# Kernel tuning notes

Hardware: AMD Instinct MI355X
Metric: run time of the kernel (lower is better)

The kernel has to match this reference:

```python
import jax, jax.numpy as jnp
import numpy as np

B, L, D = 4, 2048, 1024
H = 16
HD = D // H


def setup_inputs() -> dict:
    key = jax.random.key(0)
    ks = jax.random.split(key, 6)
    x = jax.random.normal(ks[0], (B, L, D), dtype=jnp.float32)
    # True = masked-out (strict upper triangle -> causal)
    causal_mask = jnp.triu(jnp.ones((L, L), dtype=bool), k=1)
    key_padding_mask = jnp.zeros((B, L), dtype=bool)  # no padding
    lim = 1.0 / np.sqrt(D)
    Wqkv = jax.random.uniform(ks[1], (3 * D, D), minval=-lim, maxval=lim, dtype=jnp.float32)
    bqkv = jax.random.uniform(ks[2], (3 * D,), minval=-lim, maxval=lim, dtype=jnp.float32)
    Wproj = jax.random.uniform(ks[3], (D, D), minval=-lim, maxval=lim, dtype=jnp.float32)
    bproj = jax.random.uniform(ks[4], (D,), minval=-lim, maxval=lim, dtype=jnp.float32)
    return {"x": x, "causal_mask": causal_mask, "key_padding_mask": key_padding_mask,
            "Wqkv": Wqkv, "bqkv": bqkv, "Wproj": Wproj, "bproj": bproj}


def reference(x, causal_mask, key_padding_mask, Wqkv, bqkv, Wproj, bproj):
    b, l, d = x.shape
    scale = (d // H // 1) ** 0  # placeholder; real scale below
    scale = (d // H) ** -0.5
    qkv = x @ Wqkv.T + bqkv                      # [B,L,3D]
    qkv = qkv.reshape(b, l, 3, H, HD).transpose(2, 0, 3, 1, 4)  # [3,B,H,L,HD]
    q, k, v = qkv[0], qkv[1], qkv[2]
    attn = jnp.einsum('bhqd,bhkd->bhqk', q, k) * scale          # [B,H,L,L]
    neg_inf = jnp.float32(-jnp.inf)
    attn = jnp.where(causal_mask[None, None, :, :], neg_inf, attn)
    attn = jnp.where(key_padding_mask[:, None, None, :], neg_inf, attn)
    attn = jax.nn.softmax(attn, axis=-1)
    attn = jnp.nan_to_num(attn, nan=0.0, posinf=0.0, neginf=0.0)
    out = jnp.einsum('bhqk,bhkd->bhqd', attn, v)                # [B,H,L,HD]
    out = out.transpose(0, 2, 1, 3).reshape(b, l, d)
    return out @ Wproj.T + bproj
```

## Files before the change

kernel.cpp:

```cpp
#include <hip/hip_runtime.h>

typedef __bf16 bf16;
typedef __attribute__((ext_vector_type(8))) __bf16 bf16x8;
typedef __attribute__((ext_vector_type(4))) __bf16 bf16x4;
typedef __attribute__((ext_vector_type(4))) float f32x4;
typedef __attribute__((ext_vector_type(4))) short short4v;

#define AS1C(p) ((const __attribute__((address_space(1))) void*)(p))
#define AS3(p)  ((__attribute__((address_space(3))) void*)(p))

static __device__ __forceinline__ f32x4 pv_mfma(bf16x4 a, bf16x4 b, f32x4 c) {
#if __has_builtin(__builtin_amdgcn_mfma_f32_16x16x16bf16_1k)
  return __builtin_amdgcn_mfma_f32_16x16x16bf16_1k(
      __builtin_bit_cast(short4v, a), __builtin_bit_cast(short4v, b), c, 0, 0, 0);
#else
  f32x4 d = c;
  asm("v_mfma_f32_16x16x16_bf16 %0, %1, %2, %0" : "+v"(d) : "v"(a), "v"(b));
  return d;
#endif
}

__global__ void castk(const float* __restrict__ in, bf16* __restrict__ out, long n) {
  long i = ((long)blockIdx.x * blockDim.x + threadIdx.x) * 4;
  if (i >= n) return;
  f32x4 v = *reinterpret_cast<const f32x4*>(in + i);
  bf16x4 o;
  o[0] = (bf16)v[0]; o[1] = (bf16)v[1]; o[2] = (bf16)v[2]; o[3] = (bf16)v[3];
  *reinterpret_cast<bf16x4*>(out + i) = o;
}

template<int MODE>
__global__ __launch_bounds__(256, 2)
void gemm_bt(const bf16* __restrict__ A, const bf16* __restrict__ BT,
             const float* __restrict__ bias, void* __restrict__ Cout,
             int M, int N, int K) {
  __shared__ bf16 As[128 * 64];
  __shared__ bf16 Bs[128 * 64];
  const int tid = threadIdx.x;
  const int lane = tid & 63;
  const int w = tid >> 6;
  const int wm = w >> 1, wn = w & 1;
  const int row0 = blockIdx.y * 128, col0 = blockIdx.x * 128;

  f32x4 acc[4][4] = {};

  const int srow = tid >> 3;
  const int scb = ((tid & 7) << 4) ^ ((srow & 7) << 4);
  const long aoff = (long)(row0 + srow) * K + (scb >> 1);
  const long boff = (long)(col0 + srow) * K + (scb >> 1);

  for (int k0 = 0; k0 < K; k0 += 64) {
    #pragma unroll
    for (int i = 0; i < 4; ++i) {
      __builtin_amdgcn_global_load_lds(AS1C(A + aoff + (long)i * 32 * K + k0),
                                       AS3((char*)As + i * 4096 + w * 1024), 16, 0, 0);
      __builtin_amdgcn_global_load_lds(AS1C(BT + boff + (long)i * 32 * K + k0),
                                       AS3((char*)Bs + i * 4096 + w * 1024), 16, 0, 0);
    }
    __syncthreads();
    #pragma unroll
    for (int kf = 0; kf < 2; ++kf) {
      bf16x8 af[4], bfr[4];
      #pragma unroll
      for (int m = 0; m < 4; ++m) {
        int r = wm * 64 + m * 16 + (lane & 15);
        int cb = (kf * 64 + ((lane >> 4) << 4)) ^ ((r & 7) << 4);
        af[m] = *reinterpret_cast<const bf16x8*>((const char*)As + r * 128 + cb);
      }
      #pragma unroll
      for (int n = 0; n < 4; ++n) {
        int r = wn * 64 + n * 16 + (lane & 15);
        int cb = (kf * 64 + ((lane >> 4) << 4)) ^ ((r & 7) << 4);
        bfr[n] = *reinterpret_cast<const bf16x8*>((const char*)Bs + r * 128 + cb);
      }
      #pragma unroll
      for (int m = 0; m < 4; ++m)
        #pragma unroll
        for (int n = 0; n < 4; ++n) {
          if constexpr (MODE == 1)
            acc[m][n] = __builtin_amdgcn_mfma_f32_16x16x32_bf16(bfr[n], af[m], acc[m][n], 0, 0, 0);
          else
            acc[m][n] = __builtin_amdgcn_mfma_f32_16x16x32_bf16(af[m], bfr[n], acc[m][n], 0, 0, 0);
        }
    }
    __syncthreads();
  }

  const int g = lane >> 4, q = lane & 15;

  if constexpr (MODE == 0) {
    #pragma unroll
    for (int m = 0; m < 4; ++m)
      #pragma unroll
      for (int n = 0; n < 4; ++n)
        #pragma unroll
        for (int r = 0; r < 4; ++r) {
          int grow = row0 + wm * 64 + m * 16 + g * 4 + r;
          int gcol = col0 + wn * 64 + n * 16 + q;
          reinterpret_cast<float*>(Cout)[(long)grow * N + gcol] = acc[m][n][r] + bias[gcol];
        }
  } else if constexpr (MODE == 1) {
    const int t = (int)blockIdx.x >> 3;
    const int h = (((int)blockIdx.x << 1) | wn) & 15;
    const float qs = (t == 0) ? 0.125f : 1.0f;
    bf16* outb = reinterpret_cast<bf16*>(Cout) + (t ? 8388608 : 0);
    #pragma unroll
    for (int n = 0; n < 4; ++n) {
      f32x4 bv = *reinterpret_cast<const f32x4*>(bias + col0 + wn * 64 + n * 16 + g * 4);
      #pragma unroll
      for (int m = 0; m < 4; ++m) {
        int grow = row0 + wm * 64 + m * 16 + q;
        int bb = grow >> 11, ll = grow & 2047;
        bf16x4 o;
        #pragma unroll
        for (int r = 0; r < 4; ++r) o[r] = (bf16)((acc[m][n][r] + bv[r]) * qs);
        *reinterpret_cast<bf16x4*>(outb + ((long)(bb * 16 + h) * 2048 + ll) * 64 + n * 16 + g * 4) = o;
      }
    }
  } else {
    const int h = (((int)blockIdx.x << 1) | wn) & 15;
    bf16* outb = reinterpret_cast<bf16*>(Cout);
    #pragma unroll
    for (int n = 0; n < 4; ++n) {
      float bv = bias[col0 + wn * 64 + n * 16 + q];
      int hd = n * 16 + q;
      #pragma unroll
      for (int m = 0; m < 4; ++m) {
        int grow = row0 + wm * 64 + m * 16 + g * 4;
        int bb = grow >> 11, ll = grow & 2047;
        bf16x4 o;
        #pragma unroll
        for (int r = 0; r < 4; ++r) o[r] = (bf16)(acc[m][n][r] + bv);
        *reinterpret_cast<bf16x4*>(outb + ((long)(bb * 16 + h) * 64 + hd) * 2048 + ll) = o;
      }
    }
  }
}

__global__ __launch_bounds__(256, 4)
void attn_fwd(const bf16* __restrict__ Qg, const bf16* __restrict__ Kg,
              const bf16* __restrict__ VTg, bf16* __restrict__ Og) {
  __shared__ bf16 Ks[2][64 * 64];
  __shared__ bf16 Vs[2][64 * 64];
  const int tid = threadIdx.x, lane = tid & 63, w = tid >> 6;
  const int g = lane >> 4, q = lane & 15;

  const int orig = blockIdx.x;
  const int wgid = (orig & 7) * 256 + (orig >> 3);
  const int bh = wgid >> 5;
  const int qi = 31 - (wgid & 31);
  const int bb = bh >> 4, h = bh & 15;
  const long base = (long)bh * (2048 * 64);
  const int qw = qi * 64 + w * 16;
  const int myq = qw + q;

  bf16x8 qf[2];
  qf[0] = *reinterpret_cast<const bf16x8*>(Qg + base + (long)myq * 64 + g * 8);
  qf[1] = *reinterpret_cast<const bf16x8*>(Qg + base + (long)myq * 64 + 32 + g * 8);

  f32x4 accO[4] = {};
  float m = -1e30f, l = 0.f;

  const int srow = tid >> 3;
  const int scb = ((tid & 7) << 4) ^ ((srow & 7) << 4);
  const int nt = qi + 1;

  auto stage = [&](int kt, int buf) {
    #pragma unroll
    for (int i = 0; i < 2; ++i) {
      __builtin_amdgcn_global_load_lds(
          AS1C(Kg + base + (long)(kt * 64 + i * 32 + srow) * 64 + (scb >> 1)),
          AS3((char*)&Ks[buf][0] + i * 4096 + w * 1024), 16, 0, 0);
      __builtin_amdgcn_global_load_lds(
          AS1C(VTg + base + (long)(i * 32 + srow) * 2048 + kt * 64 + (scb >> 1)),
          AS3((char*)&Vs[buf][0] + i * 4096 + w * 1024), 16, 0, 0);
    }
  };

  stage(0, 0);

  for (int kt = 0; kt < nt; ++kt) {
    const int cur = kt & 1;
    __syncthreads();
    if (kt + 1 < nt) stage(kt + 1, cur ^ 1);

    const char* Kb = (const char*)&Ks[cur][0];
    const char* Vb = (const char*)&Vs[cur][0];

    f32x4 sT[4] = {};
    #pragma unroll
    for (int kf = 0; kf < 2; ++kf) {
      #pragma unroll
      for (int a = 0; a < 4; ++a) {
        int r = a * 16 + q;
        int cb = (kf * 64 + g * 16) ^ ((r & 7) << 4);
        bf16x8 kb = *reinterpret_cast<const bf16x8*>(Kb + r * 128 + cb);
        sT[a] = __builtin_amdgcn_mfma_f32_16x16x32_bf16(kb, qf[kf], sT[a], 0, 0, 0);
      }
    }

    if (kt == qi) {
      #pragma unroll
      for (int a = 0; a < 4; ++a)
        #pragma unroll
        for (int r = 0; r < 4; ++r) {
          int kv = kt * 64 + a * 16 + 4 * g + r;
          if (kv > myq) sT[a][r] = -1e30f;
        }
    }

    float vm = -1e30f;
    #pragma unroll
    for (int a = 0; a < 4; ++a)
      #pragma unroll
      for (int r = 0; r < 4; ++r) vm = fmaxf(vm, sT[a][r]);
    vm = fmaxf(vm, __shfl_xor(vm, 16));
    vm = fmaxf(vm, __shfl_xor(vm, 32));
    float mnew = fmaxf(m, vm);
    float fac = __expf(m - mnew);
    m = mnew;

    float ps = 0.f;
    bf16x4 pa[4];
    #pragma unroll
    for (int a = 0; a < 4; ++a)
      #pragma unroll
      for (int r = 0; r < 4; ++r) {
        float p = __expf(sT[a][r] - mnew);
        ps += p;
        pa[a][r] = (bf16)p;
      }
    ps += __shfl_xor(ps, 16);
    ps += __shfl_xor(ps, 32);
    l = l * fac + ps;
    #pragma unroll
    for (int b = 0; b < 4; ++b) accO[b] *= fac;

    #pragma unroll
    for (int a = 0; a < 4; ++a) {
      #pragma unroll
      for (int b = 0; b < 4; ++b) {
        int row = b * 16 + q;
        int cb = (a * 32 + g * 8) ^ ((row & 7) << 4);
        bf16x4 vfrag = *reinterpret_cast<const bf16x4*>(Vb + row * 128 + cb);
        accO[b] = pv_mfma(vfrag, pa[a], accO[b]);
      }
    }
  }

  __syncthreads();
  char* ob = (char*)&Ks[0][0] + w * 2048;
  float rl = 1.0f / l;
  #pragma unroll
  for (int b = 0; b < 4; ++b)
    #pragma unroll
    for (int r = 0; r < 4; ++r) {
      int hd = 16 * b + 4 * g + r;
      int cb = (hd * 2) ^ ((q & 7) << 4);
      *reinterpret_cast<bf16*>(ob + q * 128 + cb) = (bf16)(accO[b][r] * rl);
    }
  asm volatile("s_waitcnt lgkmcnt(0)" ::: "memory");
  __builtin_amdgcn_sched_barrier(0);

  const int rr = lane >> 2, cc = lane & 3;
  #pragma unroll
  for (int half = 0; half < 2; ++half) {
    int hd0 = cc * 16 + half * 8;
    int cb = (hd0 * 2) ^ ((rr & 7) << 4);
    bf16x8 vv = *reinterpret_cast<const bf16x8*>(ob + rr * 128 + cb);
    *reinterpret_cast<bf16x8*>(Og + (long)(bb * 2048 + qw + rr) * 1024 + h * 64 + hd0) = vv;
  }
}

extern "C" void kernel_launch(void* const* d_in, const int* in_sizes, int n_in,
                              void* d_out, int out_size, void* d_ws, size_t ws_size,
                              hipStream_t stream) {
  (void)in_sizes; (void)n_in; (void)out_size; (void)ws_size;
  const float* x     = (const float*)d_in[0];
  const float* Wqkv  = (const float*)d_in[3];
  const float* bqkv  = (const float*)d_in[4];
  const float* Wproj = (const float*)d_in[5];
  const float* bproj = (const float*)d_in[6];

  bf16* xb     = (bf16*)d_ws;
  bf16* Wqkvb  = xb + 8388608;
  bf16* Wprojb = Wqkvb + 3145728;
  bf16* Qb     = Wprojb + 1048576;
  bf16* Ob     = Qb + 3 * 8388608;

  castk<<<8192, 256, 0, stream>>>(x, xb, 8388608);
  castk<<<3072, 256, 0, stream>>>(Wqkv, Wqkvb, 3145728);
  castk<<<1024, 256, 0, stream>>>(Wproj, Wprojb, 1048576);

  gemm_bt<1><<<dim3(16, 64), 256, 0, stream>>>(xb, Wqkvb, bqkv, (void*)Qb, 8192, 3072, 1024);
  gemm_bt<2><<<dim3(8, 64), 256, 0, stream>>>(xb, Wqkvb + (long)2048 * 1024, bqkv + 2048,
                                              (void*)(Qb + 16777216), 8192, 3072, 1024);

  attn_fwd<<<dim3(2048), 256, 0, stream>>>(Qb, Qb + 8388608, Qb + 16777216, Ob);

  gemm_bt<0><<<dim3(8, 64), 256, 0, stream>>>(Ob, Wprojb, bproj, d_out, 8192, 1024, 1024);
}
```

Baseline: 196.4 us.

## Process 128 queries per attention block with two row tiles per wave and lazy rescale

The attention kernel now handles 128 query rows per workgroup, with each wave owning two 16-row tiles that share every K/V fragment read from LDS. This halves the grid and the K/V staging traffic per query. The softmax switches to exp2 with log2(e) folded into the Q scale in the QKV GEMM, and it rescales the running max only when it grows by more than 8 (a lazy rescale). MFMA sections are wrapped in s_setprio. The cost is higher register pressure from doubled accumulators, and waves whose first tile is fully masked sit idle on the last tiles.

```diff
diff --git a/kernel.cpp b/kernel.cpp
--- a/kernel.cpp
+++ b/kernel.cpp
@@ -18,6 +18,17 @@
   asm("v_mfma_f32_16x16x16_bf16 %0, %1, %2, %0" : "+v"(d) : "v"(a), "v"(b));
   return d;
 #endif
+}
+
+static __device__ __forceinline__ float fexp2(float x) {
+#if __has_builtin(__builtin_amdgcn_exp2f)
+  return __builtin_amdgcn_exp2f(x);
+#else
+  return exp2f(x);
+#endif
+}
+static __device__ __forceinline__ float m3(float a, float b, float c) {
+  return fmaxf(fmaxf(a, b), c);
 }
 
 __global__ void castk(const float* __restrict__ in, bf16* __restrict__ out, long n) {
@@ -102,7 +113,7 @@
   } else if constexpr (MODE == 1) {
     const int t = (int)blockIdx.x >> 3;
     const int h = (((int)blockIdx.x << 1) | wn) & 15;
-    const float qs = (t == 0) ? 0.125f : 1.0f;
+    const float qs = (t == 0) ? 0.125f * 1.44269504f : 1.0f;
     bf16* outb = reinterpret_cast<bf16*>(Cout) + (t ? 8388608 : 0);
     #pragma unroll
     for (int n = 0; n < 4; ++n) {
@@ -146,24 +157,30 @@
   const int g = lane >> 4, q = lane & 15;
 
   const int orig = blockIdx.x;
-  const int wgid = (orig & 7) * 256 + (orig >> 3);
-  const int bh = wgid >> 5;
-  const int qi = 31 - (wgid & 31);
+  const int wgid = (orig & 7) * 128 + (orig >> 3);
+  const int bh = wgid >> 4;
+  const int qi = 15 - (wgid & 15);
   const int bb = bh >> 4, h = bh & 15;
   const long base = (long)bh * (2048 * 64);
-  const int qw = qi * 64 + w * 16;
-  const int myq = qw + q;
-
-  bf16x8 qf[2];
-  qf[0] = *reinterpret_cast<const bf16x8*>(Qg + base + (long)myq * 64 + g * 8);
-  qf[1] = *reinterpret_cast<const bf16x8*>(Qg + base + (long)myq * 64 + 32 + g * 8);
-
-  f32x4 accO[4] = {};
-  float m = -1e30f, l = 0.f;
+  const int q0 = qi * 128;
+  const int qw0 = q0 + w * 32, qw1 = qw0 + 16;
+  const int myq0 = qw0 + q, myq1 = qw1 + q;
+
+  const bf16* Qp = Qg + base;
+  bf16x8 qf0[2], qf1[2];
+  qf0[0] = *reinterpret_cast<const bf16x8*>(Qp + (long)myq0 * 64 + g * 8);
+  qf0[1] = *reinterpret_cast<const bf16x8*>(Qp + (long)myq0 * 64 + 32 + g * 8);
+  qf1[0] = *reinterpret_cast<const bf16x8*>(Qp + (long)myq1 * 64 + g * 8);
+  qf1[1] = *reinterpret_cast<const bf16x8*>(Qp + (long)myq1 * 64 + 32 + g * 8);
+
+  f32x4 accO0[4] = {}, accO1[4] = {};
+  float m0 = -1e30f, l0 = 0.f, m1 = -1e30f, l1 = 0.f;
 
   const int srow = tid >> 3;
   const int scb = ((tid & 7) << 4) ^ ((srow & 7) << 4);
-  const int nt = qi + 1;
+  const int nt = 2 * qi + 2;
+  const int ntw0 = ((qw0 + 15) >> 6) + 1;
+  const int ntw1 = ((qw1 + 15) >> 6) + 1;
 
   auto stage = [&](int kt, int buf) {
     #pragma unroll
@@ -177,98 +194,165 @@
     }
   };
 
+  auto osm = [&](f32x4 (&sT)[4], float& m, float& l, f32x4 (&accO)[4], bf16x4 (&pa)[4]) {
+    float t0 = m3(sT[0][0], sT[0][1], sT[0][2]);
+    float t1 = m3(sT[0][3], sT[1][0], sT[1][1]);
+    float t2 = m3(sT[1][2], sT[1][3], sT[2][0]);
+    float t3 = m3(sT[2][1], sT[2][2], sT[2][3]);
+    float t4 = m3(sT[3][0], sT[3][1], sT[3][2]);
+    float vm = fmaxf(m3(t0, t1, t2), m3(t3, t4, sT[3][3]));
+    vm = fmaxf(vm, __shfl_xor(vm, 16));
+    vm = fmaxf(vm, __shfl_xor(vm, 32));
+    if (__ballot(vm > m + 8.0f)) {
+      float mnew = fmaxf(m, vm);
+      float fac = fexp2(m - mnew);
+      m = mnew;
+      #pragma unroll
+      for (int b = 0; b < 4; ++b) accO[b] *= fac;
+      l *= fac;
+    }
+    float ps = 0.f;
+    #pragma unroll
+    for (int a = 0; a < 4; ++a)
+      #pragma unroll
+      for (int r = 0; r < 4; ++r) {
+        float p = fexp2(sT[a][r] - m);
+        ps += p;
+        pa[a][r] = (bf16)p;
+      }
+    ps += __shfl_xor(ps, 16);
+    ps += __shfl_xor(ps, 32);
+    l += ps;
+  };
+
   stage(0, 0);
 
   for (int kt = 0; kt < nt; ++kt) {
     const int cur = kt & 1;
     __syncthreads();
     if (kt + 1 < nt) stage(kt + 1, cur ^ 1);
+    if (kt >= ntw1) continue;
 
     const char* Kb = (const char*)&Ks[cur][0];
     const char* Vb = (const char*)&Vs[cur][0];
-
-    f32x4 sT[4] = {};
-    #pragma unroll
-    for (int kf = 0; kf < 2; ++kf) {
-      #pragma unroll
-      for (int a = 0; a < 4; ++a) {
-        int r = a * 16 + q;
-        int cb = (kf * 64 + g * 16) ^ ((r & 7) << 4);
-        bf16x8 kb = *reinterpret_cast<const bf16x8*>(Kb + r * 128 + cb);
-        sT[a] = __builtin_amdgcn_mfma_f32_16x16x32_bf16(kb, qf[kf], sT[a], 0, 0, 0);
-      }
-    }
-
-    if (kt == qi) {
+    const bool both = kt < ntw0;
+
+    f32x4 sT0[4] = {}, sT1[4] = {};
+    __builtin_amdgcn_s_setprio(1);
+    if (both) {
+      #pragma unroll
+      for (int kf = 0; kf < 2; ++kf)
+        #pragma unroll
+        for (int a = 0; a < 4; ++a) {
+          int r = a * 16 + q;
+          int cb = (kf * 64 + g * 16) ^ ((r & 7) << 4);
+          bf16x8 kb = *reinterpret_cast<const bf16x8*>(Kb + r * 128 + cb);
+          sT0[a] = __builtin_amdgcn_mfma_f32_16x16x32_bf16(kb, qf0[kf], sT0[a], 0, 0, 0);
+          sT1[a] = __builtin_amdgcn_mfma_f32_16x16x32_bf16(kb, qf1[kf], sT1[a], 0, 0, 0);
+        }
+    } else {
+      #pragma unroll
+      for (int kf = 0; kf < 2; ++kf)
+        #pragma unroll
+        for (int a = 0; a < 4; ++a) {
+          int r = a * 16 + q;
+          int cb = (kf * 64 + g * 16) ^ ((r & 7) << 4);
+          bf16x8 kb = *reinterpret_cast<const bf16x8*>(Kb + r * 128 + cb);
+          sT1[a] = __builtin_amdgcn_mfma_f32_16x16x32_bf16(kb, qf1[kf], sT1[a], 0, 0, 0);
+        }
+    }
+    __builtin_amdgcn_s_setprio(0);
+
+    if (kt * 64 + 63 > qw1) {
       #pragma unroll
       for (int a = 0; a < 4; ++a)
         #pragma unroll
         for (int r = 0; r < 4; ++r) {
           int kv = kt * 64 + a * 16 + 4 * g + r;
-          if (kv > myq) sT[a][r] = -1e30f;
-        }
-    }
-
-    float vm = -1e30f;
-    #pragma unroll
-    for (int a = 0; a < 4; ++a)
-      #pragma unroll
-      for (int r = 0; r < 4; ++r) vm = fmaxf(vm, sT[a][r]);
-    vm = fmaxf(vm, __shfl_xor(vm, 16));
-    vm = fmaxf(vm, __shfl_xor(vm, 32));
-    float mnew = fmaxf(m, vm);
-    float fac = __expf(m - mnew);
-    m = mnew;
-
-    float ps = 0.f;
-    bf16x4 pa[4];
-    #pragma unroll
-    for (int a = 0; a < 4; ++a)
+          if (kv > myq1) sT1[a][r] = -1e30f;
+        }
+    }
+    if (both && kt * 64 + 63 > qw0) {
+      #pragma unroll
+      for (int a = 0; a < 4; ++a)
+        #pragma unroll
+        for (int r = 0; r < 4; ++r) {
+          int kv = kt * 64 + a * 16 + 4 * g + r;
+          if (kv > myq0) sT0[a][r] = -1e30f;
+        }
+    }
+
+    bf16x4 pa0[4], pa1[4];
+    if (both) osm(sT0, m0, l0, accO0, pa0);
+    osm(sT1, m1, l1, accO1, pa1);
+
+    __builtin_amdgcn_s_setprio(1);
+    if (both) {
+      #pragma unroll
+      for (int a = 0; a < 4; ++a)
+        #pragma unroll
+        for (int b = 0; b < 4; ++b) {
+          int row = b * 16 + q;
+          int cb = (a * 32 + g * 8) ^ ((row & 7) << 4);
+          bf16x4 vfrag = *reinterpret_cast<const bf16x4*>(Vb + row * 128 + cb);
+          accO0[b] = pv_mfma(vfrag, pa0[a], accO0[b]);
+          accO1[b] = pv_mfma(vfrag, pa1[a], accO1[b]);
+        }
+    } else {
+      #pragma unroll
+      for (int a = 0; a < 4; ++a)
+        #pragma unroll
+        for (int b = 0; b < 4; ++b) {
+          int row = b * 16 + q;
+          int cb = (a * 32 + g * 8) ^ ((row & 7) << 4);
+          bf16x4 vfrag = *reinterpret_cast<const bf16x4*>(Vb + row * 128 + cb);
+          accO1[b] = pv_mfma(vfrag, pa1[a], accO1[b]);
+        }
+    }
+    __builtin_amdgcn_s_setprio(0);
+  }
+
+  __syncthreads();
+  char* lds0 = (char*)&Ks[0][0];
+  {
+    char* ob = lds0 + (w * 2 + 0) * 2048;
+    float rl = 1.0f / l0;
+    #pragma unroll
+    for (int b = 0; b < 4; ++b)
       #pragma unroll
       for (int r = 0; r < 4; ++r) {
-        float p = __expf(sT[a][r] - mnew);
-        ps += p;
-        pa[a][r] = (bf16)p;
-      }
-    ps += __shfl_xor(ps, 16);
-    ps += __shfl_xor(ps, 32);
-    l = l * fac + ps;
-    #pragma unroll
-    for (int b = 0; b < 4; ++b) accO[b] *= fac;
-
-    #pragma unroll
-    for (int a = 0; a < 4; ++a) {
-      #pragma unroll
-      for (int b = 0; b < 4; ++b) {
-        int row = b * 16 + q;
-        int cb = (a * 32 + g * 8) ^ ((row & 7) << 4);
-        bf16x4 vfrag = *reinterpret_cast<const bf16x4*>(Vb + row * 128 + cb);
-        accO[b] = pv_mfma(vfrag, pa[a], accO[b]);
-      }
-    }
-  }
-
-  __syncthreads();
-  char* ob = (char*)&Ks[0][0] + w * 2048;
-  float rl = 1.0f / l;
-  #pragma unroll
-  for (int b = 0; b < 4; ++b)
-    #pragma unroll
-    for (int r = 0; r < 4; ++r) {
-      int hd = 16 * b + 4 * g + r;
-      int cb = (hd * 2) ^ ((q & 7) << 4);
-      *reinterpret_cast<bf16*>(ob + q * 128 + cb) = (bf16)(accO[b][r] * rl);
-    }
+        int hd = 16 * b + 4 * g + r;
+        int cb = (hd * 2) ^ ((q & 7) << 4);
+        *reinterpret_cast<bf16*>(ob + q * 128 + cb) = (bf16)(accO0[b][r] * rl);
+      }
+  }
+  {
+    char* ob = lds0 + (w * 2 + 1) * 2048;
+    float rl = 1.0f / l1;
+    #pragma unroll
+    for (int b = 0; b < 4; ++b)
+      #pragma unroll
+      for (int r = 0; r < 4; ++r) {
+        int hd = 16 * b + 4 * g + r;
+        int cb = (hd * 2) ^ ((q & 7) << 4);
+        *reinterpret_cast<bf16*>(ob + q * 128 + cb) = (bf16)(accO1[b][r] * rl);
+      }
+  }
   asm volatile("s_waitcnt lgkmcnt(0)" ::: "memory");
   __builtin_amdgcn_sched_barrier(0);
 
   const int rr = lane >> 2, cc = lane & 3;
   #pragma unroll
-  for (int half = 0; half < 2; ++half) {
-    int hd0 = cc * 16 + half * 8;
-    int cb = (hd0 * 2) ^ ((rr & 7) << 4);
-    bf16x8 vv = *reinterpret_cast<const bf16x8*>(ob + rr * 128 + cb);
-    *reinterpret_cast<bf16x8*>(Og + (long)(bb * 2048 + qw + rr) * 1024 + h * 64 + hd0) = vv;
+  for (int s = 0; s < 2; ++s) {
+    char* ob = lds0 + (w * 2 + s) * 2048;
+    int qrow = qw0 + s * 16 + rr;
+    #pragma unroll
+    for (int half = 0; half < 2; ++half) {
+      int hd0 = cc * 16 + half * 8;
+      int cb = (hd0 * 2) ^ ((rr & 7) << 4);
+      bf16x8 vv = *reinterpret_cast<const bf16x8*>(ob + rr * 128 + cb);
+      *reinterpret_cast<bf16x8*>(Og + (long)(bb * 2048 + qrow) * 1024 + h * 64 + hd0) = vv;
+    }
   }
 }
 
@@ -296,7 +380,7 @@
   gemm_bt<2><<<dim3(8, 64), 256, 0, stream>>>(xb, Wqkvb + (long)2048 * 1024, bqkv + 2048,
                                               (void*)(Qb + 16777216), 8192, 3072, 1024);
 
-  attn_fwd<<<dim3(2048), 256, 0, stream>>>(Qb, Qb + 8388608, Qb + 16777216, Ob);
+  attn_fwd<<<dim3(1024), 256, 0, stream>>>(Qb, Qb + 8388608, Qb + 16777216, Ob);
 
   gemm_bt<0><<<dim3(8, 64), 256, 0, stream>>>(Ob, Wprojb, bproj, d_out, 8192, 1024, 1024);
 }
```

Measured after the change: 211.9 us. 1.08x slower.

## Share K/V tiles across 128-query attention blocks, use exp2 and lazy rescaling

Applied to the files above, without the earlier changes.

The attention kernel now runs 512-thread workgroups that cover 128 queries, so each staged K/V tile is shared by eight waves instead of four and the number of tile loads drops. Waves skip compute for tiles past their own causal limit but still take part in staging and barriers. The softmax uses exp2, with log2(e) folded into the Q scaling inside the QKV GEMM epilogue. It rescales the accumulator only when the running max rises by more than 8, and it raises wave priority around the MFMA sections and uses a three-input max tree. The launch bounds now request 8 waves per EU, which may force register pressure or spills, and idle waves on diagonal tiles add imbalance.

```diff
diff --git a/kernel.cpp b/kernel.cpp
--- a/kernel.cpp
+++ b/kernel.cpp
@@ -18,6 +18,17 @@
   asm("v_mfma_f32_16x16x16_bf16 %0, %1, %2, %0" : "+v"(d) : "v"(a), "v"(b));
   return d;
 #endif
+}
+
+static __device__ __forceinline__ float fexp2(float x) {
+#if __has_builtin(__builtin_amdgcn_exp2f)
+  return __builtin_amdgcn_exp2f(x);
+#else
+  return exp2f(x);
+#endif
+}
+static __device__ __forceinline__ float m3(float a, float b, float c) {
+  return fmaxf(fmaxf(a, b), c);
 }
 
 __global__ void castk(const float* __restrict__ in, bf16* __restrict__ out, long n) {
@@ -102,7 +113,7 @@
   } else if constexpr (MODE == 1) {
     const int t = (int)blockIdx.x >> 3;
     const int h = (((int)blockIdx.x << 1) | wn) & 15;
-    const float qs = (t == 0) ? 0.125f : 1.0f;
+    const float qs = (t == 0) ? 0.125f * 1.44269504f : 1.0f;
     bf16* outb = reinterpret_cast<bf16*>(Cout) + (t ? 8388608 : 0);
     #pragma unroll
     for (int n = 0; n < 4; ++n) {
@@ -137,7 +148,7 @@
   }
 }
 
-__global__ __launch_bounds__(256, 4)
+__global__ __launch_bounds__(512, 8)
 void attn_fwd(const bf16* __restrict__ Qg, const bf16* __restrict__ Kg,
               const bf16* __restrict__ VTg, bf16* __restrict__ Og) {
   __shared__ bf16 Ks[2][64 * 64];
@@ -146,12 +157,13 @@
   const int g = lane >> 4, q = lane & 15;
 
   const int orig = blockIdx.x;
-  const int wgid = (orig & 7) * 256 + (orig >> 3);
-  const int bh = wgid >> 5;
-  const int qi = 31 - (wgid & 31);
+  const int wgid = (orig & 7) * 128 + (orig >> 3);
+  const int bh = wgid >> 4;
+  const int qi = 15 - (wgid & 15);
   const int bb = bh >> 4, h = bh & 15;
   const long base = (long)bh * (2048 * 64);
-  const int qw = qi * 64 + w * 16;
+  const int q0 = qi * 128;
+  const int qw = q0 + w * 16;
   const int myq = qw + q;
 
   bf16x8 qf[2];
@@ -163,18 +175,16 @@
 
   const int srow = tid >> 3;
   const int scb = ((tid & 7) << 4) ^ ((srow & 7) << 4);
-  const int nt = qi + 1;
+  const int nt = 2 * qi + 2;
+  const int ntw = (qw >> 6) + 1;
 
   auto stage = [&](int kt, int buf) {
-    #pragma unroll
-    for (int i = 0; i < 2; ++i) {
-      __builtin_amdgcn_global_load_lds(
-          AS1C(Kg + base + (long)(kt * 64 + i * 32 + srow) * 64 + (scb >> 1)),
-          AS3((char*)&Ks[buf][0] + i * 4096 + w * 1024), 16, 0, 0);
-      __builtin_amdgcn_global_load_lds(
-          AS1C(VTg + base + (long)(i * 32 + srow) * 2048 + kt * 64 + (scb >> 1)),
-          AS3((char*)&Vs[buf][0] + i * 4096 + w * 1024), 16, 0, 0);
-    }
+    __builtin_amdgcn_global_load_lds(
+        AS1C(Kg + base + (long)(kt * 64 + srow) * 64 + (scb >> 1)),
+        AS3((char*)&Ks[buf][0] + tid * 16), 16, 0, 0);
+    __builtin_amdgcn_global_load_lds(
+        AS1C(VTg + base + (long)srow * 2048 + kt * 64 + (scb >> 1)),
+        AS3((char*)&Vs[buf][0] + tid * 16), 16, 0, 0);
   };
 
   stage(0, 0);
@@ -183,13 +193,15 @@
     const int cur = kt & 1;
     __syncthreads();
     if (kt + 1 < nt) stage(kt + 1, cur ^ 1);
+    if (kt >= ntw) continue;
 
     const char* Kb = (const char*)&Ks[cur][0];
     const char* Vb = (const char*)&Vs[cur][0];
 
     f32x4 sT[4] = {};
-    #pragma unroll
-    for (int kf = 0; kf < 2; ++kf) {
+    __builtin_amdgcn_s_setprio(1);
+    #pragma unroll
+    for (int kf = 0; kf < 2; ++kf)
       #pragma unroll
       for (int a = 0; a < 4; ++a) {
         int r = a * 16 + q;
@@ -197,9 +209,9 @@
         bf16x8 kb = *reinterpret_cast<const bf16x8*>(Kb + r * 128 + cb);
         sT[a] = __builtin_amdgcn_mfma_f32_16x16x32_bf16(kb, qf[kf], sT[a], 0, 0, 0);
       }
-    }
-
-    if (kt == qi) {
+    __builtin_amdgcn_s_setprio(0);
+
+    if (kt == ntw - 1) {
       #pragma unroll
       for (int a = 0; a < 4; ++a)
         #pragma unroll
@@ -209,35 +221,41 @@
         }
     }
 
-    float vm = -1e30f;
-    #pragma unroll
-    for (int a = 0; a < 4; ++a)
-      #pragma unroll
-      for (int r = 0; r < 4; ++r) vm = fmaxf(vm, sT[a][r]);
-    vm = fmaxf(vm, __shfl_xor(vm, 16));
-    vm = fmaxf(vm, __shfl_xor(vm, 32));
-    float mnew = fmaxf(m, vm);
-    float fac = __expf(m - mnew);
-    m = mnew;
-
+    {
+      float t0 = m3(sT[0][0], sT[0][1], sT[0][2]);
+      float t1 = m3(sT[0][3], sT[1][0], sT[1][1]);
+      float t2 = m3(sT[1][2], sT[1][3], sT[2][0]);
+      float t3 = m3(sT[2][1], sT[2][2], sT[2][3]);
+      float t4 = m3(sT[3][0], sT[3][1], sT[3][2]);
+      float vm = fmaxf(m3(t0, t1, t2), m3(t3, t4, sT[3][3]));
+      vm = fmaxf(vm, __shfl_xor(vm, 16));
+      vm = fmaxf(vm, __shfl_xor(vm, 32));
+      if (__ballot(vm > m + 8.0f)) {
+        float mnew = fmaxf(m, vm);
+        float fac = fexp2(m - mnew);
+        m = mnew;
+        #pragma unroll
+        for (int b = 0; b < 4; ++b) accO[b] *= fac;
+        l *= fac;
+      }
+    }
     float ps = 0.f;
     bf16x4 pa[4];
     #pragma unroll
     for (int a = 0; a < 4; ++a)
       #pragma unroll
       for (int r = 0; r < 4; ++r) {
-        float p = __expf(sT[a][r] - mnew);
+        float p = fexp2(sT[a][r] - m);
         ps += p;
         pa[a][r] = (bf16)p;
       }
     ps += __shfl_xor(ps, 16);
     ps += __shfl_xor(ps, 32);
-    l = l * fac + ps;
-    #pragma unroll
-    for (int b = 0; b < 4; ++b) accO[b] *= fac;
-
-    #pragma unroll
-    for (int a = 0; a < 4; ++a) {
+    l += ps;
+
+    __builtin_amdgcn_s_setprio(1);
+    #pragma unroll
+    for (int a = 0; a < 4; ++a)
       #pragma unroll
       for (int b = 0; b < 4; ++b) {
         int row = b * 16 + q;
@@ -245,7 +263,7 @@
         bf16x4 vfrag = *reinterpret_cast<const bf16x4*>(Vb + row * 128 + cb);
         accO[b] = pv_mfma(vfrag, pa[a], accO[b]);
       }
-    }
+    __builtin_amdgcn_s_setprio(0);
   }
 
   __syncthreads();
@@ -296,7 +314,7 @@
   gemm_bt<2><<<dim3(8, 64), 256, 0, stream>>>(xb, Wqkvb + (long)2048 * 1024, bqkv + 2048,
                                               (void*)(Qb + 16777216), 8192, 3072, 1024);
 
-  attn_fwd<<<dim3(2048), 256, 0, stream>>>(Qb, Qb + 8388608, Qb + 16777216, Ob);
+  attn_fwd<<<dim3(1024), 512, 0, stream>>>(Qb, Qb + 8388608, Qb + 16777216, Ob);
 
   gemm_bt<0><<<dim3(8, 64), 256, 0, stream>>>(Ob, Wprojb, bproj, d_out, 8192, 1024, 1024);
 }
```

Result: slower. 215.7 us (+9.8%).

## Triple-buffer K/V staging with vmcnt waits and use exp2 softmax

Applied to the files above, without the earlier changes.

The attention kernel moves from double to triple buffering of K/V tiles in LDS, prefetching two tiles ahead and replacing the full __syncthreads with an explicit vmcnt wait plus s_barrier. The softmax uses native exp2 with log2(e) folded into the Q scale in the QKV GEMM epilogue, and the row max uses three-input max trees. This aims to hide global-load latency and trim softmax ALU work, at the cost of more LDS per block (possibly lower occupancy) and redundant dummy loads near the tail.

```diff
diff --git a/kernel.cpp b/kernel.cpp
--- a/kernel.cpp
+++ b/kernel.cpp
@@ -18,6 +18,17 @@
   asm("v_mfma_f32_16x16x16_bf16 %0, %1, %2, %0" : "+v"(d) : "v"(a), "v"(b));
   return d;
 #endif
+}
+
+static __device__ __forceinline__ float fexp2(float x) {
+#if __has_builtin(__builtin_amdgcn_exp2f)
+  return __builtin_amdgcn_exp2f(x);
+#else
+  return exp2f(x);
+#endif
+}
+static __device__ __forceinline__ float m3(float a, float b, float c) {
+  return fmaxf(fmaxf(a, b), c);
 }
 
 __global__ void castk(const float* __restrict__ in, bf16* __restrict__ out, long n) {
@@ -102,7 +113,7 @@
   } else if constexpr (MODE == 1) {
     const int t = (int)blockIdx.x >> 3;
     const int h = (((int)blockIdx.x << 1) | wn) & 15;
-    const float qs = (t == 0) ? 0.125f : 1.0f;
+    const float qs = (t == 0) ? 0.125f * 1.44269504f : 1.0f;
     bf16* outb = reinterpret_cast<bf16*>(Cout) + (t ? 8388608 : 0);
     #pragma unroll
     for (int n = 0; n < 4; ++n) {
@@ -140,19 +151,20 @@
 __global__ __launch_bounds__(256, 4)
 void attn_fwd(const bf16* __restrict__ Qg, const bf16* __restrict__ Kg,
               const bf16* __restrict__ VTg, bf16* __restrict__ Og) {
-  __shared__ bf16 Ks[2][64 * 64];
-  __shared__ bf16 Vs[2][64 * 64];
+  __shared__ bf16 Ks[3][64 * 64];
+  __shared__ bf16 Vs[3][64 * 64];
   const int tid = threadIdx.x, lane = tid & 63, w = tid >> 6;
   const int g = lane >> 4, q = lane & 15;
 
   const int orig = blockIdx.x;
   const int wgid = (orig & 7) * 256 + (orig >> 3);
   const int bh = wgid >> 5;
-  const int qi = 31 - (wgid & 31);
+  const int qt = 31 - (wgid & 31);
   const int bb = bh >> 4, h = bh & 15;
   const long base = (long)bh * (2048 * 64);
-  const int qw = qi * 64 + w * 16;
+  const int qw = qt * 64 + w * 16;
   const int myq = qw + q;
+  const int nt = qt + 1;
 
   bf16x8 qf[2];
   qf[0] = *reinterpret_cast<const bf16x8*>(Qg + base + (long)myq * 64 + g * 8);
@@ -163,7 +175,6 @@
 
   const int srow = tid >> 3;
   const int scb = ((tid & 7) << 4) ^ ((srow & 7) << 4);
-  const int nt = qi + 1;
 
   auto stage = [&](int kt, int buf) {
     #pragma unroll
@@ -178,11 +189,16 @@
   };
 
   stage(0, 0);
+  stage(nt > 1 ? 1 : 0, 1);
+  asm volatile("" ::: "memory");
 
   for (int kt = 0; kt < nt; ++kt) {
-    const int cur = kt & 1;
-    __syncthreads();
-    if (kt + 1 < nt) stage(kt + 1, cur ^ 1);
+    const int cur = kt % 3;
+    asm volatile("s_waitcnt vmcnt(4)" ::: "memory");
+    __builtin_amdgcn_s_barrier();
+    { int nk = kt + 2 < nt ? kt + 2 : nt - 1;
+      stage(nk, (kt + 2) % 3); }
+    asm volatile("" ::: "memory");
 
     const char* Kb = (const char*)&Ks[cur][0];
     const char* Vb = (const char*)&Vs[cur][0];
@@ -199,7 +215,7 @@
       }
     }
 
-    if (kt == qi) {
+    if (kt == qt) {
       #pragma unroll
       for (int a = 0; a < 4; ++a)
         #pragma unroll
@@ -209,15 +225,16 @@
         }
     }
 
-    float vm = -1e30f;
-    #pragma unroll
-    for (int a = 0; a < 4; ++a)
-      #pragma unroll
-      for (int r = 0; r < 4; ++r) vm = fmaxf(vm, sT[a][r]);
+    float t0 = m3(sT[0][0], sT[0][1], sT[0][2]);
+    float t1 = m3(sT[0][3], sT[1][0], sT[1][1]);
+    float t2 = m3(sT[1][2], sT[1][3], sT[2][0]);
+    float t3 = m3(sT[2][1], sT[2][2], sT[2][3]);
+    float t4 = m3(sT[3][0], sT[3][1], sT[3][2]);
+    float vm = fmaxf(m3(t0, t1, t2), m3(t3, t4, sT[3][3]));
     vm = fmaxf(vm, __shfl_xor(vm, 16));
     vm = fmaxf(vm, __shfl_xor(vm, 32));
     float mnew = fmaxf(m, vm);
-    float fac = __expf(m - mnew);
+    float fac = fexp2(m - mnew);
     m = mnew;
 
     float ps = 0.f;
@@ -226,7 +243,7 @@
     for (int a = 0; a < 4; ++a)
       #pragma unroll
       for (int r = 0; r < 4; ++r) {
-        float p = __expf(sT[a][r] - mnew);
+        float p = fexp2(sT[a][r] - mnew);
         ps += p;
         pa[a][r] = (bf16)p;
       }
@@ -248,6 +265,7 @@
     }
   }
 
+  asm volatile("s_waitcnt vmcnt(0)" ::: "memory");
   __syncthreads();
   char* ob = (char*)&Ks[0][0] + w * 2048;
   float rl = 1.0f / l;
```

Measured after the change: 201.4 us. 1.03x slower.
